# Kernel tuning notes

Measured on AMD Instinct MI355X. Metric: run time of the kernel, lower is better.

## Reference

```python
import math
import jax, jax.numpy as jnp
import numpy as np

B, S, D, H = 512, 128, 128, 8


def setup_inputs() -> dict:
    key = jax.random.key(0)
    ks = jax.random.split(key, 12)
    u = 1.0 / D
    return {
        "encoded_inputs": jax.random.normal(ks[0], (B, S, D), jnp.float32) * 0.1,
        "locations": jax.random.uniform(ks[1], (B, S, 2), jnp.float32),
        "scores": jax.random.uniform(ks[2], (B, S), jnp.float32),
        "Tmax": jax.random.uniform(ks[3], (B,), jnp.float32, minval=2.0, maxval=4.0),
        "m": jax.random.randint(ks[4], (B,), 1, 6, jnp.int32),
        # parameters (nn.Linear(in,out,bias=False) stored as [in,out] for x @ W)
        "W_ctx": jax.random.uniform(ks[5], (D, D), jnp.float32, -u, u),
        "W_upd": jax.random.uniform(ks[6], (3 * D, D), jnp.float32, -u, u),
        "W_nodes": jax.random.uniform(ks[7], (D, 3 * D), jnp.float32, -u, u),
        "W_out": jax.random.uniform(ks[8], (D, D), jnp.float32, -u, u),
        "vtmax": jax.random.uniform(ks[9], (D,), jnp.float32, -u, u),
        "vm": jax.random.uniform(ks[10], (D,), jnp.float32, -u, u),
        "W_placeholder": jax.random.uniform(ks[11], (D,), jnp.float32, -1.0, 1.0),
    }


def reference(encoded_inputs, locations, scores, Tmax, m,
              W_ctx, W_upd, W_nodes, W_out, vtmax, vm, W_placeholder):
    Bb, Ss, Dd = encoded_inputs.shape
    n_head = H
    dk = Dd // n_head
    C = 10.0
    EPS = 1e-12  # grad-safe sqrt; distances between random points are >0 a.s.

    # geometry (computed once, as in torch forward)
    diff = locations[:, :, None, :] - locations[:, None, :, :]
    dists = jnp.sqrt(jnp.sum(diff * diff, -1) + EPS)            # [B,S,S]
    d2depot = jnp.sqrt(jnp.sum((locations - locations[:, 0:1]) ** 2, -1) + EPS)  # [B,S]

    # fixed context + node projections (torch recomputes these every step; same math hoisted)
    h_hat = jnp.mean(encoded_inputs, 1) @ W_ctx                  # [B,D]
    kvl = encoded_inputs @ W_nodes                               # [B,S,3D]
    gK, gV, logK = jnp.split(kvl, 3, axis=-1)
    gK = gK.reshape(Bb, Ss, n_head, dk)
    gV = gV.reshape(Bb, Ss, n_head, dk)

    b_idx = jnp.arange(Bb)
    TMAX0 = Tmax
    mask0 = jnp.zeros((Bb, Ss), bool).at[:, :2].set(True)
    carry0 = (mask0, Tmax, m, jnp.ones(Bb, bool),
              jnp.zeros(Bb, jnp.int32), jnp.zeros(Bb, jnp.float32), jnp.int32(0))

    def step(carry, _):
        mask, Tm, mm, start, last, total, t = carry
        etmax = Tm[:, None] * vtmax[None, :]                     # [B,D]
        em = mm.astype(jnp.float32)[:, None] * vm[None, :]       # [B,D]
        gathered = encoded_inputs[b_idx, last]                   # [B,D]
        mylast = jnp.where(t == 0, W_placeholder[None, :], gathered)
        embft = jnp.concatenate([mylast, etmax, em], -1)         # [B,3D]
        query = h_hat + embft @ W_upd                            # [B,D]
        q = query.reshape(Bb, n_head, dk)
        compat = jnp.einsum('bhd,bshd->bhs', q, gK) / math.sqrt(dk)
        compat = jnp.where(mask[:, None, :], -jnp.inf, compat)
        attn = jax.nn.softmax(compat, -1)
        heads = jnp.einsum('bhs,bshd->bhd', attn, gV).reshape(Bb, Dd)
        glimpse = heads @ W_out                                  # [B,D]
        logits = jnp.einsum('bd,bsd->bs', glimpse, logK) / math.sqrt(Dd)
        logits = jnp.tanh(logits) * C
        logits = jnp.where(mask, -jnp.inf, logits)
        logits = jax.nn.log_softmax(logits, -1)                  # [B,S]
        city = jnp.argmax(logits, -1).astype(jnp.int32)          # greedy decode

        d_lc = dists[b_idx, last, city]
        d_cd = d2depot[b_idx, city]
        d_lc = jnp.where(start, d_cd, d_lc)
        is_valid = d_lc + d_cd <= Tm
        Tm = jnp.where(is_valid, Tm - d_lc, Tm)
        start = jnp.where(is_valid & start, False, start)
        total = total + jnp.where(is_valid, scores[b_idx, city], 0.0)
        d_lo = dists[b_idx, last, 1:]                            # old last, [B,S-1]
        greater = d_lo + d2depot[:, 1:] > Tm[:, None]
        all_g = jnp.all(greater | mask[:, 1:], -1)
        double = all_g & (mm - 1 > 0)
        mm = jnp.where(double, mm - 1, mm)
        start = start | double
        Tm = jnp.where(double, TMAX0, Tm)
        last = jnp.where(is_valid, city, last)
        mask = mask.at[b_idx, city].set(True)
        return (mask, Tm, mm, start, last, total, t + 1), (logits, city)

    (_, _, _, _, _, totalScore, _), (logits_seq, cities) = jax.lax.scan(
        step, carry0, None, length=Ss - 2)
    solution = cities.T                                          # [B,T]
    log_p = jnp.take_along_axis(jnp.transpose(logits_seq, (1, 0, 2)),
                                solution[:, :, None], 2).squeeze(-1)
    log_probabilities = log_p.sum(-1)                            # [B]
    return (log_probabilities, totalScore, solution)
```

## Files before the change

### kernel.cpp

```cpp
#include <hip/hip_runtime.h>
#include <math.h>

#define NB 512
#define SS 128
#define DD 128
#define NH 8
#define DKK 16
#define NSTEP 126

__global__ __launch_bounds__(128) void proj_kernel(
    const float* __restrict__ vtmax, const float* __restrict__ vm,
    const float* __restrict__ wplc, const float* __restrict__ Wupd,
    float* __restrict__ wtp, float* __restrict__ wmp, float* __restrict__ plcq)
{
  int d = threadIdx.x;
  double a = 0.0, b = 0.0, c = 0.0;
  for (int k = 0; k < DD; k++) {
    a += (double)vtmax[k] * (double)Wupd[(size_t)(DD + k) * DD + d];
    b += (double)vm[k]    * (double)Wupd[(size_t)(2 * DD + k) * DD + d];
    c += (double)wplc[k]  * (double)Wupd[(size_t)k * DD + d];
  }
  wtp[d] = (float)a; wmp[d] = (float)b; plcq[d] = (float)c;
}

__global__ __launch_bounds__(128) void hhat_kernel(
    const float* __restrict__ enc, const float* __restrict__ Wctx,
    float* __restrict__ hh)
{
  __shared__ double mean[DD];
  int b = blockIdx.x, d = threadIdx.x;
  double s = 0.0;
  for (int j = 0; j < SS; j++) s += (double)enc[((size_t)b * SS + j) * DD + d];
  mean[d] = s * (1.0 / 128.0);
  __syncthreads();
  double a = 0.0;
  for (int k = 0; k < DD; k++) a += mean[k] * (double)Wctx[(size_t)k * DD + d];
  hh[(size_t)b * DD + d] = (float)a;
}

__global__ __launch_bounds__(256) void gemm64(
    const float* __restrict__ A, const float* __restrict__ Bm, int ldb,
    float* __restrict__ C, int ldc)
{
  __shared__ float As[64][132];
  __shared__ float Bs[64][68];
  const int r0 = blockIdx.x * 64;
  const int c0 = blockIdx.y * 64;
  const int tid = threadIdx.x;
  #pragma unroll
  for (int i = 0; i < 8; i++) {
    int idx = tid + 256 * i;
    int rr = idx >> 5;
    int cc = (idx & 31) << 2;
    *(float4*)&As[rr][cc] = *(const float4*)&A[(size_t)(r0 + rr) * DD + cc];
  }
  const int trow = (tid >> 4) << 2;
  const int tcol = (tid & 15) << 2;
  double acc[4][4] = {};
  for (int kh = 0; kh < 2; kh++) {
    __syncthreads();
    #pragma unroll
    for (int i = 0; i < 4; i++) {
      int idx = tid + 256 * i;
      int rr = idx >> 4;
      int cc = (idx & 15) << 2;
      *(float4*)&Bs[rr][cc] = *(const float4*)&Bm[(size_t)(kh * 64 + rr) * ldb + c0 + cc];
    }
    __syncthreads();
    #pragma unroll 2
    for (int k2 = 0; k2 < 64; k2++) {
      int k = kh * 64 + k2;
      double a0 = (double)As[trow][k],     a1 = (double)As[trow + 1][k],
             a2 = (double)As[trow + 2][k], a3 = (double)As[trow + 3][k];
      float4 b4 = *(const float4*)&Bs[k2][tcol];
      double bx = (double)b4.x, by = (double)b4.y, bz = (double)b4.z, bw = (double)b4.w;
      acc[0][0] += a0 * bx; acc[0][1] += a0 * by; acc[0][2] += a0 * bz; acc[0][3] += a0 * bw;
      acc[1][0] += a1 * bx; acc[1][1] += a1 * by; acc[1][2] += a1 * bz; acc[1][3] += a1 * bw;
      acc[2][0] += a2 * bx; acc[2][1] += a2 * by; acc[2][2] += a2 * bz; acc[2][3] += a2 * bw;
      acc[3][0] += a3 * bx; acc[3][1] += a3 * by; acc[3][2] += a3 * bz; acc[3][3] += a3 * bw;
    }
  }
  #pragma unroll
  for (int i = 0; i < 4; i++) {
    float* cp = &C[(size_t)(r0 + trow + i) * ldc + c0 + tcol];
    cp[0] = (float)acc[i][0]; cp[1] = (float)acc[i][1];
    cp[2] = (float)acc[i][2]; cp[3] = (float)acc[i][3];
  }
}

template<bool USE_ENCU>
__global__ __launch_bounds__(256) void decoder_kernel(
    const float* __restrict__ loc, const float* __restrict__ scores,
    const float* __restrict__ Tmax, const int* __restrict__ m_in,
    const float* __restrict__ Wout, const float* __restrict__ Wupd,
    const float* __restrict__ enc,
    const float* __restrict__ kvl, const float* __restrict__ encU,
    const float* __restrict__ hhat,
    const float* __restrict__ wtp, const float* __restrict__ wmp,
    const float* __restrict__ plcq, float* __restrict__ out)
{
  const int b = blockIdx.x;
  const int tid = threadIdx.x;
  const int wv = tid >> 6, ln = tid & 63;

  __shared__ float lx[SS], lyv[SS], d2dep[SS], sc[SS];
  __shared__ float qv[DD];
  __shared__ float comp[NH][SS];
  __shared__ double hpart[2][DD];
  __shared__ float headsv[DD];
  __shared__ float gl[DD];
  __shared__ float lg[SS];
  __shared__ float shv[SS];
  __shared__ float encrow[DD];
  __shared__ int maskv[SS];
  __shared__ float redf[4];
  __shared__ double redd[4];
  __shared__ float redy[2]; __shared__ int redyi[2];
  __shared__ int redi[4];
  __shared__ int bc_city;
  __shared__ float s_Tm, s_T0, s_total;
  __shared__ double s_logp;
  __shared__ int s_last, s_mm, s_start, s_isv, s_startA;

  if (tid < SS) {
    lx[tid]  = loc[((size_t)b * SS + tid) * 2];
    lyv[tid] = loc[((size_t)b * SS + tid) * 2 + 1];
    sc[tid]  = scores[(size_t)b * SS + tid];
    maskv[tid] = (tid < 2) ? 1 : 0;
  }
  if (tid == 0) {
    s_Tm = Tmax[b]; s_T0 = Tmax[b]; s_mm = m_in[b];
    s_start = 1; s_last = 0; s_total = 0.f; s_logp = 0.0;
  }
  __syncthreads();
  if (tid < SS) {
    float dx = __fsub_rn(lx[tid], lx[0]), dy = __fsub_rn(lyv[tid], lyv[0]);
    d2dep[tid] = __fsqrt_rn(__fadd_rn(__fadd_rn(__fmul_rn(dx, dx), __fmul_rn(dy, dy)), 1e-12f));
  }
  float hh_r = 0.f, wtp_r = 0.f, wmp_r = 0.f, plcq_r = 0.f;
  if (tid < DD) {
    hh_r = hhat[(size_t)b * DD + tid];
    wtp_r = wtp[tid]; wmp_r = wmp[tid]; plcq_r = plcq[tid];
  }

  for (int t = 0; t < NSTEP; t++) {
    __syncthreads();
    if (!USE_ENCU) {
      if (t > 0 && tid < DD)
        encrow[tid] = enc[((size_t)b * SS + s_last) * DD + tid];
      __syncthreads();
    }
    if (tid < DD) {
      double acc = (double)hh_r + (double)s_Tm * (double)wtp_r + (double)s_mm * (double)wmp_r;
      if (t == 0) {
        acc += (double)plcq_r;
      } else if (USE_ENCU) {
        acc += (double)encU[((size_t)b * SS + s_last) * DD + tid];
      } else {
        double s0 = 0.0;
        for (int k = 0; k < DD; k++) s0 += (double)encrow[k] * (double)Wupd[(size_t)k * DD + tid];
        acc += s0;
      }
      qv[tid] = (float)acc;
    }
    __syncthreads();
    #pragma unroll
    for (int i = 0; i < 4; i++) {
      int p = tid + 256 * i;
      int h = p >> 7, s = p & 127;
      const float* kp = kvl + ((size_t)(b * SS + s)) * 384 + h * DKK;
      const float* qh = qv + h * DKK;
      double c = 0.0;
      #pragma unroll
      for (int j = 0; j < 16; j++) c += (double)kp[j] * (double)qh[j];
      comp[h][s] = maskv[s] ? -INFINITY : __fmul_rn((float)c, 0.25f);
    }
    __syncthreads();
    #pragma unroll
    for (int hh2 = 0; hh2 < 2; hh2++) {
      int h = wv * 2 + hh2;
      float a0 = comp[h][ln], a1 = comp[h][ln + 64];
      float mx = fmaxf(a0, a1);
      #pragma unroll
      for (int off = 32; off > 0; off >>= 1) mx = fmaxf(mx, __shfl_xor(mx, off));
      float e0 = expf(__fsub_rn(a0, mx)), e1 = expf(__fsub_rn(a1, mx));
      double sm = (double)e0 + (double)e1;
      #pragma unroll
      for (int off = 32; off > 0; off >>= 1) sm += __shfl_xor(sm, off);
      float sumf = (float)sm;
      comp[h][ln]      = __fdiv_rn(e0, sumf);
      comp[h][ln + 64] = __fdiv_rn(e1, sumf);
    }
    __syncthreads();
    {
      int di = tid & 15, h = (tid >> 4) & 7, p = tid >> 7;
      const float* vp = kvl + (size_t)b * SS * 384 + 128 + h * DKK + di;
      double acc = 0.0;
      int sbase = p * 64;
      #pragma unroll 8
      for (int s2 = 0; s2 < 64; s2++)
        acc += (double)comp[h][sbase + s2] * (double)vp[(size_t)(sbase + s2) * 384];
      hpart[p][tid & 127] = acc;
    }
    __syncthreads();
    if (tid < DD) headsv[tid] = (float)(hpart[0][tid] + hpart[1][tid]);
    __syncthreads();
    if (tid < DD) {
      double a = 0.0;
      #pragma unroll 8
      for (int k = 0; k < DD; k++) a += (double)headsv[k] * (double)Wout[(size_t)k * DD + tid];
      gl[tid] = (float)a;
    }
    __syncthreads();
    if (tid < SS) {
      const float* lk = kvl + ((size_t)(b * SS + tid)) * 384 + 256;
      double a = 0.0;
      #pragma unroll 8
      for (int k = 0; k < DD; k++) a += (double)lk[k] * (double)gl[k];
      float dotf = (float)a;
      float z = __fdiv_rn(dotf, 11.313708498984761f);
      float l = __fmul_rn(tanhf(z), 10.0f);
      lg[tid] = maskv[tid] ? -INFINITY : l;
    }
    __syncthreads();
    if (tid < 128) {
      float mv = lg[tid];
      #pragma unroll
      for (int off = 32; off > 0; off >>= 1) mv = fmaxf(mv, __shfl_xor(mv, off));
      if (ln == 0) redf[wv] = mv;
    }
    __syncthreads();
    float Lq = (float)log((double)(NSTEP - t));
    if (tid < 128) {
      float mx128 = fmaxf(redf[0], redf[1]);
      float sh = __fsub_rn(lg[tid], mx128);
      shv[tid] = sh;
      float yv = __fsub_rn(sh, Lq); int yi = tid;
      #pragma unroll
      for (int off = 32; off > 0; off >>= 1) {
        float ov = __shfl_xor(yv, off); int oi = __shfl_xor(yi, off);
        if (ov > yv || (ov == yv && oi < yi)) { yv = ov; yi = oi; }
      }
      if (ln == 0) { redy[wv] = yv; redyi[wv] = yi; }
      double e = exp((double)sh);
      #pragma unroll
      for (int off = 32; off > 0; off >>= 1) e += __shfl_xor(e, off);
      if (ln == 0) redd[wv] = e;
    }
    __syncthreads();
    if (tid == 0) {
      float yv = redy[0]; int yi = redyi[0];
      if (redy[1] > yv || (redy[1] == yv && redyi[1] < yi)) { yv = redy[1]; yi = redyi[1]; }
      bc_city = yi;
      double sumexp = redd[0] + redd[1];
      s_logp += (double)shv[yi] - log(sumexp);
      int city = yi;
      float dx = __fsub_rn(lx[s_last], lx[city]), dy = __fsub_rn(lyv[s_last], lyv[city]);
      float d_lc = __fsqrt_rn(__fadd_rn(__fadd_rn(__fmul_rn(dx, dx), __fmul_rn(dy, dy)), 1e-12f));
      float d_cd = d2dep[city];
      if (s_start) d_lc = d_cd;
      int isv = (__fadd_rn(d_lc, d_cd) <= s_Tm) ? 1 : 0;
      if (isv) { s_Tm = __fsub_rn(s_Tm, d_lc); s_total = __fadd_rn(s_total, sc[city]); }
      s_isv = isv;
      s_startA = (isv && s_start) ? 0 : s_start;
      out[1024 + (size_t)b * NSTEP + t] = (float)city;
    }
    __syncthreads();
    if (tid < 128) {
      int g = 1;
      if (tid >= 1) {
        float dx = __fsub_rn(lx[s_last], lx[tid]), dy = __fsub_rn(lyv[s_last], lyv[tid]);
        float dlo = __fsqrt_rn(__fadd_rn(__fadd_rn(__fmul_rn(dx, dx), __fmul_rn(dy, dy)), 1e-12f));
        g = ((__fadd_rn(dlo, d2dep[tid]) > s_Tm) || maskv[tid]) ? 1 : 0;
      }
      int aw = __all(g);
      if (ln == 0) redi[wv] = aw;
    }
    __syncthreads();
    if (tid == 0) {
      int all_g = redi[0] && redi[1];
      int dbl = (all_g && (s_mm - 1 > 0)) ? 1 : 0;
      if (dbl) { s_mm -= 1; s_Tm = s_T0; }
      s_start = (s_startA || dbl) ? 1 : 0;
      if (s_isv) s_last = bc_city;
      maskv[bc_city] = 1;
    }
  }
  __syncthreads();
  if (tid == 0) {
    out[b] = (float)s_logp;
    out[512 + b] = s_total;
  }
}

extern "C" void kernel_launch(void* const* d_in, const int* in_sizes, int n_in,
                              void* d_out, int out_size, void* d_ws, size_t ws_size,
                              hipStream_t stream) {
  const float* enc    = (const float*)d_in[0];
  const float* loc    = (const float*)d_in[1];
  const float* scores = (const float*)d_in[2];
  const float* Tmax   = (const float*)d_in[3];
  const int*   m_in   = (const int*)d_in[4];
  const float* W_ctx  = (const float*)d_in[5];
  const float* W_upd  = (const float*)d_in[6];
  const float* W_nodes= (const float*)d_in[7];
  const float* W_out  = (const float*)d_in[8];
  const float* vtmax  = (const float*)d_in[9];
  const float* vm     = (const float*)d_in[10];
  const float* Wplc   = (const float*)d_in[11];
  float* out = (float*)d_out;
  float* ws  = (float*)d_ws;

  float* kvl  = ws;
  float* hhat = kvl + 25165824;
  float* wtp  = hhat + 65536;
  float* wmp  = wtp + 128;
  float* plcq = wmp + 128;
  float* encU = plcq + 128;

  const size_t need_base = (size_t)(25165824 + 65536 + 384) * 4;
  const size_t need_full = need_base + (size_t)8388608 * 4;
  const bool use_encu = ws_size >= need_full;

  proj_kernel<<<dim3(1), dim3(128), 0, stream>>>(vtmax, vm, Wplc, W_upd, wtp, wmp, plcq);
  hhat_kernel<<<dim3(NB), dim3(128), 0, stream>>>(enc, W_ctx, hhat);
  gemm64<<<dim3(1024, 6), dim3(256), 0, stream>>>(enc, W_nodes, 384, kvl, 384);
  if (use_encu) {
    gemm64<<<dim3(1024, 2), dim3(256), 0, stream>>>(enc, W_upd, 128, encU, 128);
    decoder_kernel<true><<<dim3(NB), dim3(256), 0, stream>>>(loc, scores, Tmax, m_in, W_out, W_upd, enc,
                                                             kvl, encU, hhat, wtp, wmp, plcq, out);
  } else {
    decoder_kernel<false><<<dim3(NB), dim3(256), 0, stream>>>(loc, scores, Tmax, m_in, W_out, W_upd, enc,
                                                              kvl, (const float*)nullptr, hhat, wtp, wmp, plcq, out);
  }
}
```

Measured before the change: 2.302 ms.

## Stage node K/logit-K in LDS and V/Wout slices in registers across decode steps

Before the 126-step decode loop, each block loads the per-batch glimpse-K and logit-K projections transposed into padded shared memory, and holds its V column slice and Wout slice in registers. Each step then reads these from on-chip storage instead of re-reading global memory. The Wout and logit matvecs are split across all 256 threads with partial sums and four independent accumulators. The cost is about 130KB of LDS plus 128 extra registers per thread, forcing one block per CU (launch_bounds 256,1) and risking spills. Summation order changes slightly.

```diff
diff --git a/kernel.cpp b/kernel.cpp
--- a/kernel.cpp
+++ b/kernel.cpp
@@ -89,7 +89,7 @@
 }
 
 template<bool USE_ENCU>
-__global__ __launch_bounds__(256) void decoder_kernel(
+__global__ __launch_bounds__(256, 1) void decoder_kernel(
     const float* __restrict__ loc, const float* __restrict__ scores,
     const float* __restrict__ Tmax, const int* __restrict__ m_in,
     const float* __restrict__ Wout, const float* __restrict__ Wupd,
@@ -103,12 +103,14 @@
   const int tid = threadIdx.x;
   const int wv = tid >> 6, ln = tid & 63;
 
+  __shared__ float gKT[DD][129];
+  __shared__ float lKT[DD][129];
   __shared__ float lx[SS], lyv[SS], d2dep[SS], sc[SS];
-  __shared__ float qv[DD];
+  __shared__ double qv_d[DD];
   __shared__ float comp[NH][SS];
   __shared__ double hpart[2][DD];
-  __shared__ float headsv[DD];
-  __shared__ float gl[DD];
+  __shared__ double headsd[DD];
+  __shared__ double gld[DD];
   __shared__ float lg[SS];
   __shared__ float shv[SS];
   __shared__ float encrow[DD];
@@ -122,6 +124,35 @@
   __shared__ double s_logp;
   __shared__ int s_last, s_mm, s_start, s_isv, s_startA;
 
+  const float* kb_ = kvl + (size_t)b * SS * 384;
+
+  #pragma unroll
+  for (int it = 0; it < 16; ++it) {
+    int idx = tid + 256 * it;
+    int s = idx >> 5;
+    int c4 = (idx & 31) << 2;
+    float4 vk = *(const float4*)(kb_ + (size_t)s * 384 + c4);
+    float4 vl = *(const float4*)(kb_ + (size_t)s * 384 + 256 + c4);
+    gKT[c4 + 0][s] = vk.x; gKT[c4 + 1][s] = vk.y;
+    gKT[c4 + 2][s] = vk.z; gKT[c4 + 3][s] = vk.w;
+    lKT[c4 + 0][s] = vl.x; lKT[c4 + 1][s] = vl.y;
+    lKT[c4 + 2][s] = vl.z; lKT[c4 + 3][s] = vl.w;
+  }
+  float gvreg[64];
+  {
+    int c = tid & 127, sbase = (tid >> 7) * 64;
+    #pragma unroll
+    for (int j = 0; j < 64; ++j)
+      gvreg[j] = kb_[(size_t)(sbase + j) * 384 + 128 + c];
+  }
+  float woreg[64];
+  {
+    int d = tid & 127, kbse = (tid >> 7) * 64;
+    #pragma unroll
+    for (int j = 0; j < 64; ++j)
+      woreg[j] = Wout[(size_t)(kbse + j) * DD + d];
+  }
+
   if (tid < SS) {
     lx[tid]  = loc[((size_t)b * SS + tid) * 2];
     lyv[tid] = loc[((size_t)b * SS + tid) * 2 + 1];
@@ -161,18 +192,18 @@
         for (int k = 0; k < DD; k++) s0 += (double)encrow[k] * (double)Wupd[(size_t)k * DD + tid];
         acc += s0;
       }
-      qv[tid] = (float)acc;
+      float qf = (float)acc;
+      qv_d[tid] = (double)qf;
     }
     __syncthreads();
     #pragma unroll
     for (int i = 0; i < 4; i++) {
       int p = tid + 256 * i;
       int h = p >> 7, s = p & 127;
-      const float* kp = kvl + ((size_t)(b * SS + s)) * 384 + h * DKK;
-      const float* qh = qv + h * DKK;
+      const double* qh = qv_d + h * DKK;
       double c = 0.0;
       #pragma unroll
-      for (int j = 0; j < 16; j++) c += (double)kp[j] * (double)qh[j];
+      for (int j = 0; j < 16; j++) c += (double)gKT[h * DKK + j][s] * qh[j];
       comp[h][s] = maskv[s] ? -INFINITY : __fmul_rn((float)c, 0.25f);
     }
     __syncthreads();
@@ -193,31 +224,51 @@
     }
     __syncthreads();
     {
-      int di = tid & 15, h = (tid >> 4) & 7, p = tid >> 7;
-      const float* vp = kvl + (size_t)b * SS * 384 + 128 + h * DKK + di;
-      double acc = 0.0;
+      int h = (tid >> 4) & 7, p = tid >> 7;
       int sbase = p * 64;
-      #pragma unroll 8
-      for (int s2 = 0; s2 < 64; s2++)
-        acc += (double)comp[h][sbase + s2] * (double)vp[(size_t)(sbase + s2) * 384];
-      hpart[p][tid & 127] = acc;
-    }
-    __syncthreads();
-    if (tid < DD) headsv[tid] = (float)(hpart[0][tid] + hpart[1][tid]);
-    __syncthreads();
-    if (tid < DD) {
-      double a = 0.0;
-      #pragma unroll 8
-      for (int k = 0; k < DD; k++) a += (double)headsv[k] * (double)Wout[(size_t)k * DD + tid];
-      gl[tid] = (float)a;
+      double a0 = 0.0, a1 = 0.0, a2 = 0.0, a3 = 0.0;
+      #pragma unroll
+      for (int j = 0; j < 64; j += 4) {
+        a0 += (double)comp[h][sbase + j]     * (double)gvreg[j];
+        a1 += (double)comp[h][sbase + j + 1] * (double)gvreg[j + 1];
+        a2 += (double)comp[h][sbase + j + 2] * (double)gvreg[j + 2];
+        a3 += (double)comp[h][sbase + j + 3] * (double)gvreg[j + 3];
+      }
+      hpart[p][tid & 127] = (a0 + a1) + (a2 + a3);
+    }
+    __syncthreads();
+    if (tid < DD) headsd[tid] = (double)(float)(hpart[0][tid] + hpart[1][tid]);
+    __syncthreads();
+    {
+      int d = tid & 127, kb2 = (tid >> 7) * 64;
+      double a0 = 0.0, a1 = 0.0, a2 = 0.0, a3 = 0.0;
+      #pragma unroll
+      for (int j = 0; j < 64; j += 4) {
+        a0 += headsd[kb2 + j]     * (double)woreg[j];
+        a1 += headsd[kb2 + j + 1] * (double)woreg[j + 1];
+        a2 += headsd[kb2 + j + 2] * (double)woreg[j + 2];
+        a3 += headsd[kb2 + j + 3] * (double)woreg[j + 3];
+      }
+      hpart[tid >> 7][d] = (a0 + a1) + (a2 + a3);
+    }
+    __syncthreads();
+    if (tid < DD) gld[tid] = (double)(float)(hpart[0][tid] + hpart[1][tid]);
+    __syncthreads();
+    {
+      int s = tid & 127, kb2 = (tid >> 7) * 64;
+      double a0 = 0.0, a1 = 0.0, a2 = 0.0, a3 = 0.0;
+      #pragma unroll
+      for (int j = 0; j < 64; j += 4) {
+        a0 += (double)lKT[kb2 + j][s]     * gld[kb2 + j];
+        a1 += (double)lKT[kb2 + j + 1][s] * gld[kb2 + j + 1];
+        a2 += (double)lKT[kb2 + j + 2][s] * gld[kb2 + j + 2];
+        a3 += (double)lKT[kb2 + j + 3][s] * gld[kb2 + j + 3];
+      }
+      hpart[tid >> 7][s] = (a0 + a1) + (a2 + a3);
     }
     __syncthreads();
     if (tid < SS) {
-      const float* lk = kvl + ((size_t)(b * SS + tid)) * 384 + 256;
-      double a = 0.0;
-      #pragma unroll 8
-      for (int k = 0; k < DD; k++) a += (double)lk[k] * (double)gl[k];
-      float dotf = (float)a;
+      float dotf = (float)(hpart[0][tid] + hpart[1][tid]);
       float z = __fdiv_rn(dotf, 11.313708498984761f);
       float l = __fmul_rn(tanhf(z), 10.0f);
       lg[tid] = maskv[tid] ? -INFINITY : l;
```

Result: slower. 2.411 ms (+4.7%).
